# Optimization experiments

Measured on AMD Instinct MI355X. Metric: run time of the kernel, lower is better.

Reference implementation:

```python
import jax, jax.numpy as jnp
import numpy as np

H = 1024        # hidden_size
V = 50257       # output_size (vocab)
L = 2048        # max_length (encoder sequence)


def setup_inputs() -> dict:
    key = jax.random.key(0)
    ks = jax.random.split(key, 10)
    s = 1.0 / np.sqrt(H)
    return {
        "input_tok": jax.random.randint(ks[0], (1,), 0, V),
        "hidden": jax.random.normal(ks[1], (2, 1, H), dtype=jnp.float32),
        "encoder_hiddens": jax.random.normal(ks[2], (L, H), dtype=jnp.float32),
        # learned parameters
        "emb": jax.random.normal(ks[3], (V, H), dtype=jnp.float32),
        "W_ih": jax.random.uniform(ks[4], (2, H, H), jnp.float32, -s, s),   # per-direction input weights
        "W_hh": jax.random.uniform(ks[5], (2, H, H), jnp.float32, -s, s),   # per-direction recurrent weights
        "b_ih": jax.random.uniform(ks[6], (2, H), jnp.float32, -s, s),
        "b_hh": jax.random.uniform(ks[7], (2, H), jnp.float32, -s, s),
        "W_out": jax.random.uniform(ks[8], (V, 4 * H), jnp.float32, -s, s),
        "b_out": jax.random.uniform(ks[9], (V,), jnp.float32, -s, s),
    }


def reference(input_tok, hidden, encoder_hiddens, emb, W_ih, W_hh, b_ih, b_hh, W_out, b_out):
    # embedding lookup -> (H,)  (dropout is identity in eval mode)
    x = emb[input_tok[0]]
    # single-step bidirectional vanilla RNN cell (both directions see the same x):
    # h' = tanh(x W_ih^T + b_ih + h0 W_hh^T + b_hh), per direction d in {fwd, bwd}
    h0 = hidden[:, 0, :]                                    # (2, H)
    h = jnp.tanh(jnp.einsum('dho,o->dh', W_ih, x) + b_ih
                 + jnp.einsum('dho,do->dh', W_hh, h0) + b_hh)  # (2, H)
    # dot-product attention per direction over encoder states (L, H)
    energy = jnp.einsum('dh,lh->dl', h, encoder_hiddens)    # (2, L)
    attn = jax.nn.softmax(energy, axis=-1)                  # (2, L)
    attn_out = jnp.einsum('dl,lh->dh', attn, encoder_hiddens)  # (2, H)
    # concat: (attn_fwd, h_fwd, attn_bwd, h_bwd) -> (1, 4H)
    concat = jnp.concatenate([attn_out[0], h[0], attn_out[1], h[1]])[None, :]
    logits = concat @ W_out.T + b_out                       # (1, V)
    output = jax.nn.log_softmax(logits, axis=1)
    return output, h[:, None, :]                            # ((1, V), (2, 1, H))
```

## Files before the change

### kernel.cpp

```cpp
#include <hip/hip_runtime.h>
#include <cmath>

#define HDIM 1024
#define LSEQ 2048
#define VOCAB 50257

__device__ __forceinline__ float wave_sum(float v) {
#pragma unroll
    for (int off = 32; off; off >>= 1) v += __shfl_down(v, off, 64);
    return v;
}

__device__ __forceinline__ float wave_max(float v) {
#pragma unroll
    for (int off = 32; off; off >>= 1) v = fmaxf(v, __shfl_down(v, off, 64));
    return v;
}

__device__ __forceinline__ void lse_combine(float& m, float& s, float m2, float s2) {
    float nm = fmaxf(m, m2);
    s = s * expf(m - nm) + s2 * expf(m2 - nm);
    m = nm;
}

__global__ void rnn_kernel(const int* __restrict__ tok,
                           const float* __restrict__ hidden,
                           const float* __restrict__ emb,
                           const float* __restrict__ W_ih,
                           const float* __restrict__ W_hh,
                           const float* __restrict__ b_ih,
                           const float* __restrict__ b_hh,
                           float* __restrict__ concat,
                           float* __restrict__ out_h) {
    int wave = threadIdx.x >> 6, lane = threadIdx.x & 63;
    int row = blockIdx.x * 4 + wave;
    int d = row >> 10, i = row & 1023;
    int t = tok[0];
    const float* x  = emb + (size_t)t * HDIM;
    const float* h0 = hidden + d * HDIM;
    const float* wi = W_ih + (size_t)d * HDIM * HDIM + (size_t)i * HDIM;
    const float* wh = W_hh + (size_t)d * HDIM * HDIM + (size_t)i * HDIM;
    float acc = 0.f;
#pragma unroll
    for (int p = 0; p < 4; ++p) {
        int o = p * 256 + lane * 4;
        float4 a = *(const float4*)(wi + o);
        float4 b = *(const float4*)(x + o);
        acc += a.x * b.x + a.y * b.y + a.z * b.z + a.w * b.w;
        float4 c = *(const float4*)(wh + o);
        float4 e = *(const float4*)(h0 + o);
        acc += c.x * e.x + c.y * e.y + c.z * e.z + c.w * e.w;
    }
    acc = wave_sum(acc);
    if (lane == 0) {
        float hv = tanhf(acc + b_ih[d * HDIM + i] + b_hh[d * HDIM + i]);
        concat[d * 2048 + 1024 + i] = hv;
        out_h[d * HDIM + i] = hv;
    }
}

__global__ void energy_kernel(const float* __restrict__ enc,
                              const float* __restrict__ concat,
                              float* __restrict__ energy) {
    int wave = threadIdx.x >> 6, lane = threadIdx.x & 63;
    int row = blockIdx.x * 4 + wave;
    int d = row >> 11, l = row & 2047;
    const float* h  = concat + d * 2048 + 1024;
    const float* er = enc + (size_t)l * HDIM;
    float acc = 0.f;
#pragma unroll
    for (int p = 0; p < 4; ++p) {
        int o = p * 256 + lane * 4;
        float4 a = *(const float4*)(er + o);
        float4 b = *(const float4*)(h + o);
        acc += a.x * b.x + a.y * b.y + a.z * b.z + a.w * b.w;
    }
    acc = wave_sum(acc);
    if (lane == 0) energy[row] = acc;
}

__global__ void softmax_kernel(const float* __restrict__ energy,
                               float* __restrict__ attnw) {
    __shared__ float red[4];
    int d = blockIdx.x, t = threadIdx.x;
    int lane = t & 63, wave = t >> 6;
    const float* e = energy + d * LSEQ;
    float vals[8];
    float m = -1e30f;
#pragma unroll
    for (int k = 0; k < 8; ++k) { vals[k] = e[t + 256 * k]; m = fmaxf(m, vals[k]); }
    m = wave_max(m);
    if (lane == 0) red[wave] = m;
    __syncthreads();
    m = fmaxf(fmaxf(red[0], red[1]), fmaxf(red[2], red[3]));
    __syncthreads();
    float s = 0.f;
#pragma unroll
    for (int k = 0; k < 8; ++k) { vals[k] = expf(vals[k] - m); s += vals[k]; }
    s = wave_sum(s);
    if (lane == 0) red[wave] = s;
    __syncthreads();
    s = red[0] + red[1] + red[2] + red[3];
    float inv = 1.f / s;
#pragma unroll
    for (int k = 0; k < 8; ++k) attnw[d * LSEQ + t + 256 * k] = vals[k] * inv;
}

__global__ void attnout_partial_kernel(const float* __restrict__ enc,
                                       const float* __restrict__ attnw,
                                       float* __restrict__ part) {
    int b = blockIdx.x;
    int d = b >> 5, c = b & 31;
    int t = threadIdx.x;
    float acc0 = 0, acc1 = 0, acc2 = 0, acc3 = 0;
    const float* aw = attnw + d * LSEQ + c * 64;
    const float* e  = enc + (size_t)(c * 64) * HDIM;
    for (int l = 0; l < 64; ++l) {
        float a = aw[l];
        const float* row = e + (size_t)l * HDIM;
        acc0 += a * row[t];
        acc1 += a * row[t + 256];
        acc2 += a * row[t + 512];
        acc3 += a * row[t + 768];
    }
    float* pp = part + (size_t)b * HDIM;
    pp[t] = acc0; pp[t + 256] = acc1; pp[t + 512] = acc2; pp[t + 768] = acc3;
}

__global__ void attnout_reduce_kernel(const float* __restrict__ part,
                                      float* __restrict__ concat) {
    int idx = blockIdx.x * 256 + threadIdx.x;
    int d = idx >> 10, h = idx & 1023;
    float s = 0.f;
#pragma unroll 8
    for (int c = 0; c < 32; ++c) s += part[(size_t)(d * 32 + c) * HDIM + h];
    concat[d * 2048 + h] = s;
}

__global__ void logits_kernel(const float* __restrict__ W_out,
                              const float* __restrict__ b_out,
                              const float* __restrict__ concat,
                              float* __restrict__ logits) {
    int wave = threadIdx.x >> 6, lane = threadIdx.x & 63;
    int v = blockIdx.x * 4 + wave;
    if (v >= VOCAB) return;
    const float* w = W_out + (size_t)v * 4096;
    float acc = 0.f;
#pragma unroll
    for (int p = 0; p < 16; ++p) {
        int o = p * 256 + lane * 4;
        float4 a = *(const float4*)(w + o);
        float4 b = *(const float4*)(concat + o);
        acc += a.x * b.x + a.y * b.y + a.z * b.z + a.w * b.w;
    }
    acc = wave_sum(acc);
    if (lane == 0) logits[v] = acc + b_out[v];
}

__global__ void lse_partial_kernel(const float* __restrict__ logits,
                                   float* __restrict__ pm,
                                   float* __restrict__ ps) {
    __shared__ float rm[4], rs[4];
    int tid = blockIdx.x * 256 + threadIdx.x;
    float m = -1e30f, s = 0.f;
    for (int v = tid; v < VOCAB; v += 128 * 256) lse_combine(m, s, logits[v], 1.f);
    int lane = threadIdx.x & 63, wave = threadIdx.x >> 6;
#pragma unroll
    for (int off = 32; off; off >>= 1) {
        float m2 = __shfl_down(m, off, 64);
        float s2 = __shfl_down(s, off, 64);
        lse_combine(m, s, m2, s2);
    }
    if (lane == 0) { rm[wave] = m; rs[wave] = s; }
    __syncthreads();
    if (threadIdx.x == 0) {
        float fm = rm[0], fs = rs[0];
        for (int w = 1; w < 4; ++w) lse_combine(fm, fs, rm[w], rs[w]);
        pm[blockIdx.x] = fm;
        ps[blockIdx.x] = fs;
    }
}

__global__ void lse_final_kernel(const float* __restrict__ pm,
                                 const float* __restrict__ ps,
                                 float* __restrict__ Mval) {
    int lane = threadIdx.x;
    float m = pm[lane], s = ps[lane];
    lse_combine(m, s, pm[lane + 64], ps[lane + 64]);
#pragma unroll
    for (int off = 32; off; off >>= 1) {
        float m2 = __shfl_down(m, off, 64);
        float s2 = __shfl_down(s, off, 64);
        lse_combine(m, s, m2, s2);
    }
    if (lane == 0) Mval[0] = m + logf(s);
}

__global__ void sub_kernel(const float* __restrict__ logits,
                           const float* __restrict__ Mval,
                           float* __restrict__ out) {
    int v = blockIdx.x * 256 + threadIdx.x;
    if (v < VOCAB) out[v] = logits[v] - Mval[0];
}

extern "C" void kernel_launch(void* const* d_in, const int* in_sizes, int n_in,
                              void* d_out, int out_size, void* d_ws, size_t ws_size,
                              hipStream_t stream) {
    const int*   tok    = (const int*)d_in[0];
    const float* hidden = (const float*)d_in[1];
    const float* enc    = (const float*)d_in[2];
    const float* emb    = (const float*)d_in[3];
    const float* W_ih   = (const float*)d_in[4];
    const float* W_hh   = (const float*)d_in[5];
    const float* b_ih   = (const float*)d_in[6];
    const float* b_hh   = (const float*)d_in[7];
    const float* W_out  = (const float*)d_in[8];
    const float* b_out  = (const float*)d_in[9];
    float* out = (float*)d_out;

    float* ws     = (float*)d_ws;
    float* concat = ws;
    float* energy = ws + 4096;
    float* attnw  = ws + 8192;
    float* logits = ws + 12288;
    float* pm     = ws + 62592;
    float* ps     = ws + 62720;
    float* Mval   = ws + 62848;
    float* part   = ws + 62912;

    rnn_kernel<<<512, 256, 0, stream>>>(tok, hidden, emb, W_ih, W_hh, b_ih, b_hh,
                                        concat, out + VOCAB);
    energy_kernel<<<1024, 256, 0, stream>>>(enc, concat, energy);
    softmax_kernel<<<2, 256, 0, stream>>>(energy, attnw);
    attnout_partial_kernel<<<64, 256, 0, stream>>>(enc, attnw, part);
    attnout_reduce_kernel<<<8, 256, 0, stream>>>(part, concat);
    logits_kernel<<<(VOCAB + 3) / 4, 256, 0, stream>>>(W_out, b_out, concat, logits);
    lse_partial_kernel<<<128, 256, 0, stream>>>(logits, pm, ps);
    lse_final_kernel<<<1, 64, 0, stream>>>(pm, ps, Mval);
    sub_kernel<<<(VOCAB + 255) / 256, 256, 0, stream>>>(logits, Mval, out);
}
```

Baseline: 162.4 us.

## Fuse attention into flash-style split softmax and fold log-softmax reductions into logits

Replaces the separate energy, softmax, weighted-sum and reduce kernels with a chunked flash-attention kernel that computes local max/sum and unnormalised partial outputs, followed by a rescaling combine kernel. The logits kernel now also emits per-block max and exp-sum. A single output kernel has each block redundantly reduce those partials and subtract the log-sum-exp. This cuts the launch count and the intermediate buffer traffic, at the cost of redundant global LSE reduction in every output block.

Result: slower. 183.5 us (+13.0%).

```diff
diff --git a/kernel.cpp b/kernel.cpp
--- a/kernel.cpp
+++ b/kernel.cpp
@@ -4,16 +4,11 @@
 #define HDIM 1024
 #define LSEQ 2048
 #define VOCAB 50257
+#define LOGIT_BLOCKS ((VOCAB + 3) / 4)
 
 __device__ __forceinline__ float wave_sum(float v) {
 #pragma unroll
     for (int off = 32; off; off >>= 1) v += __shfl_down(v, off, 64);
-    return v;
-}
-
-__device__ __forceinline__ float wave_max(float v) {
-#pragma unroll
-    for (int off = 32; off; off >>= 1) v = fmaxf(v, __shfl_down(v, off, 64));
     return v;
 }
 
@@ -59,92 +54,83 @@
     }
 }
 
-__global__ void energy_kernel(const float* __restrict__ enc,
-                              const float* __restrict__ concat,
-                              float* __restrict__ energy) {
-    int wave = threadIdx.x >> 6, lane = threadIdx.x & 63;
-    int row = blockIdx.x * 4 + wave;
-    int d = row >> 11, l = row & 2047;
-    const float* h  = concat + d * 2048 + 1024;
-    const float* er = enc + (size_t)l * HDIM;
-    float acc = 0.f;
-#pragma unroll
-    for (int p = 0; p < 4; ++p) {
-        int o = p * 256 + lane * 4;
-        float4 a = *(const float4*)(er + o);
-        float4 b = *(const float4*)(h + o);
-        acc += a.x * b.x + a.y * b.y + a.z * b.z + a.w * b.w;
-    }
-    acc = wave_sum(acc);
-    if (lane == 0) energy[row] = acc;
-}
-
-__global__ void softmax_kernel(const float* __restrict__ energy,
-                               float* __restrict__ attnw) {
-    __shared__ float red[4];
-    int d = blockIdx.x, t = threadIdx.x;
-    int lane = t & 63, wave = t >> 6;
-    const float* e = energy + d * LSEQ;
-    float vals[8];
-    float m = -1e30f;
-#pragma unroll
-    for (int k = 0; k < 8; ++k) { vals[k] = e[t + 256 * k]; m = fmaxf(m, vals[k]); }
-    m = wave_max(m);
-    if (lane == 0) red[wave] = m;
-    __syncthreads();
-    m = fmaxf(fmaxf(red[0], red[1]), fmaxf(red[2], red[3]));
-    __syncthreads();
-    float s = 0.f;
-#pragma unroll
-    for (int k = 0; k < 8; ++k) { vals[k] = expf(vals[k] - m); s += vals[k]; }
-    s = wave_sum(s);
-    if (lane == 0) red[wave] = s;
-    __syncthreads();
-    s = red[0] + red[1] + red[2] + red[3];
-    float inv = 1.f / s;
-#pragma unroll
-    for (int k = 0; k < 8; ++k) attnw[d * LSEQ + t + 256 * k] = vals[k] * inv;
-}
-
-__global__ void attnout_partial_kernel(const float* __restrict__ enc,
-                                       const float* __restrict__ attnw,
-                                       float* __restrict__ part) {
+__global__ void flash_attn_kernel(const float* __restrict__ enc,
+                                  const float* __restrict__ concat,
+                                  float* __restrict__ part,
+                                  float* __restrict__ pm_a,
+                                  float* __restrict__ ps_a) {
+    __shared__ float e_sh[32];
     int b = blockIdx.x;
-    int d = b >> 5, c = b & 31;
-    int t = threadIdx.x;
+    int d = b >> 6, c = b & 63;
+    int t = threadIdx.x, wave = t >> 6, lane = t & 63;
+    int base = c * 32;
+    const float* h = concat + d * 2048 + 1024;
+
+    for (int r = 0; r < 8; ++r) {
+        int ll = wave * 8 + r;
+        const float* er = enc + (size_t)(base + ll) * HDIM;
+        float acc = 0.f;
+#pragma unroll
+        for (int p = 0; p < 4; ++p) {
+            int o = p * 256 + lane * 4;
+            float4 a = *(const float4*)(er + o);
+            float4 bb = *(const float4*)(h + o);
+            acc += a.x * bb.x + a.y * bb.y + a.z * bb.z + a.w * bb.w;
+        }
+        acc = wave_sum(acc);
+        if (lane == 0) e_sh[ll] = acc;
+    }
+    __syncthreads();
+
+    float m_c = -1e30f;
+#pragma unroll
+    for (int l = 0; l < 32; ++l) m_c = fmaxf(m_c, e_sh[l]);
+    float s_c = 0.f;
     float acc0 = 0, acc1 = 0, acc2 = 0, acc3 = 0;
-    const float* aw = attnw + d * LSEQ + c * 64;
-    const float* e  = enc + (size_t)(c * 64) * HDIM;
-    for (int l = 0; l < 64; ++l) {
-        float a = aw[l];
-        const float* row = e + (size_t)l * HDIM;
-        acc0 += a * row[t];
-        acc1 += a * row[t + 256];
-        acc2 += a * row[t + 512];
-        acc3 += a * row[t + 768];
+    for (int l = 0; l < 32; ++l) {
+        float p = expf(e_sh[l] - m_c);
+        s_c += p;
+        const float* row = enc + (size_t)(base + l) * HDIM;
+        acc0 += p * row[t];
+        acc1 += p * row[t + 256];
+        acc2 += p * row[t + 512];
+        acc3 += p * row[t + 768];
     }
     float* pp = part + (size_t)b * HDIM;
     pp[t] = acc0; pp[t + 256] = acc1; pp[t + 512] = acc2; pp[t + 768] = acc3;
-}
-
-__global__ void attnout_reduce_kernel(const float* __restrict__ part,
-                                      float* __restrict__ concat) {
+    if (t == 0) { pm_a[b] = m_c; ps_a[b] = s_c; }
+}
+
+__global__ void attn_combine_kernel(const float* __restrict__ part,
+                                    const float* __restrict__ pm_a,
+                                    const float* __restrict__ ps_a,
+                                    float* __restrict__ concat) {
     int idx = blockIdx.x * 256 + threadIdx.x;
     int d = idx >> 10, h = idx & 1023;
-    float s = 0.f;
-#pragma unroll 8
-    for (int c = 0; c < 32; ++c) s += part[(size_t)(d * 32 + c) * HDIM + h];
-    concat[d * 2048 + h] = s;
+    float M = -1e30f;
+    for (int c = 0; c < 64; ++c) M = fmaxf(M, pm_a[d * 64 + c]);
+    float S = 0.f, acc = 0.f;
+    for (int c = 0; c < 64; ++c) {
+        int cb = d * 64 + c;
+        float w = expf(pm_a[cb] - M);
+        S += ps_a[cb] * w;
+        acc += part[(size_t)cb * HDIM + h] * w;
+    }
+    concat[d * 2048 + h] = acc / S;
 }
 
 __global__ void logits_kernel(const float* __restrict__ W_out,
                               const float* __restrict__ b_out,
                               const float* __restrict__ concat,
-                              float* __restrict__ logits) {
+                              float* __restrict__ logits,
+                              float* __restrict__ pm,
+                              float* __restrict__ ps) {
+    __shared__ float lv[4];
     int wave = threadIdx.x >> 6, lane = threadIdx.x & 63;
     int v = blockIdx.x * 4 + wave;
-    if (v >= VOCAB) return;
-    const float* w = W_out + (size_t)v * 4096;
+    bool valid = v < VOCAB;
+    int vc = valid ? v : (VOCAB - 1);
+    const float* w = W_out + (size_t)vc * 4096;
     float acc = 0.f;
 #pragma unroll
     for (int p = 0; p < 16; ++p) {
@@ -154,17 +140,31 @@
         acc += a.x * b.x + a.y * b.y + a.z * b.z + a.w * b.w;
     }
     acc = wave_sum(acc);
-    if (lane == 0) logits[v] = acc + b_out[v];
-}
-
-__global__ void lse_partial_kernel(const float* __restrict__ logits,
-                                   float* __restrict__ pm,
-                                   float* __restrict__ ps) {
-    __shared__ float rm[4], rs[4];
-    int tid = blockIdx.x * 256 + threadIdx.x;
+    if (lane == 0) {
+        float val = acc + b_out[vc];
+        if (valid) logits[v] = val;
+        lv[wave] = valid ? val : -1e30f;
+    }
+    __syncthreads();
+    if (threadIdx.x == 0) {
+        float m = fmaxf(fmaxf(lv[0], lv[1]), fmaxf(lv[2], lv[3]));
+        float s = 0.f;
+#pragma unroll
+        for (int k = 0; k < 4; ++k)
+            if (lv[k] > -1e29f) s += expf(lv[k] - m);
+        pm[blockIdx.x] = m;
+        ps[blockIdx.x] = s;
+    }
+}
+
+__global__ void out_kernel(const float* __restrict__ logits,
+                           const float* __restrict__ pm,
+                           const float* __restrict__ ps,
+                           float* __restrict__ out) {
+    __shared__ float rm[4], rs[4], Msh;
+    int t = threadIdx.x, lane = t & 63, wave = t >> 6;
     float m = -1e30f, s = 0.f;
-    for (int v = tid; v < VOCAB; v += 128 * 256) lse_combine(m, s, logits[v], 1.f);
-    int lane = threadIdx.x & 63, wave = threadIdx.x >> 6;
+    for (int i = t; i < LOGIT_BLOCKS; i += 256) lse_combine(m, s, pm[i], ps[i]);
 #pragma unroll
     for (int off = 32; off; off >>= 1) {
         float m2 = __shfl_down(m, off, 64);
@@ -173,34 +173,15 @@
     }
     if (lane == 0) { rm[wave] = m; rs[wave] = s; }
     __syncthreads();
-    if (threadIdx.x == 0) {
+    if (t == 0) {
         float fm = rm[0], fs = rs[0];
-        for (int w = 1; w < 4; ++w) lse_combine(fm, fs, rm[w], rs[w]);
-        pm[blockIdx.x] = fm;
-        ps[blockIdx.x] = fs;
-    }
-}
-
-__global__ void lse_final_kernel(const float* __restrict__ pm,
-                                 const float* __restrict__ ps,
-                                 float* __restrict__ Mval) {
-    int lane = threadIdx.x;
-    float m = pm[lane], s = ps[lane];
-    lse_combine(m, s, pm[lane + 64], ps[lane + 64]);
-#pragma unroll
-    for (int off = 32; off; off >>= 1) {
-        float m2 = __shfl_down(m, off, 64);
-        float s2 = __shfl_down(s, off, 64);
-        lse_combine(m, s, m2, s2);
-    }
-    if (lane == 0) Mval[0] = m + logf(s);
-}
-
-__global__ void sub_kernel(const float* __restrict__ logits,
-                           const float* __restrict__ Mval,
-                           float* __restrict__ out) {
-    int v = blockIdx.x * 256 + threadIdx.x;
-    if (v < VOCAB) out[v] = logits[v] - Mval[0];
+        for (int k = 1; k < 4; ++k) lse_combine(fm, fs, rm[k], rs[k]);
+        Msh = fm + logf(fs);
+    }
+    __syncthreads();
+    float M = Msh;
+    int v = blockIdx.x * 256 + t;
+    if (v < VOCAB) out[v] = logits[v] - M;
 }
 
 extern "C" void kernel_launch(void* const* d_in, const int* in_sizes, int n_in,
@@ -220,22 +201,17 @@
 
     float* ws     = (float*)d_ws;
     float* concat = ws;
-    float* energy = ws + 4096;
-    float* attnw  = ws + 8192;
-    float* logits = ws + 12288;
-    float* pm     = ws + 62592;
-    float* ps     = ws + 62720;
-    float* Mval   = ws + 62848;
-    float* part   = ws + 62912;
+    float* pm_a   = ws + 4096;
+    float* ps_a   = ws + 4224;
+    float* pm     = ws + 4352;
+    float* ps     = ws + 16928;
+    float* part   = ws + 29504;
+    float* logits = ws + 29504;
 
     rnn_kernel<<<512, 256, 0, stream>>>(tok, hidden, emb, W_ih, W_hh, b_ih, b_hh,
                                         concat, out + VOCAB);
-    energy_kernel<<<1024, 256, 0, stream>>>(enc, concat, energy);
-    softmax_kernel<<<2, 256, 0, stream>>>(energy, attnw);
-    attnout_partial_kernel<<<64, 256, 0, stream>>>(enc, attnw, part);
-    attnout_reduce_kernel<<<8, 256, 0, stream>>>(part, concat);
-    logits_kernel<<<(VOCAB + 3) / 4, 256, 0, stream>>>(W_out, b_out, concat, logits);
-    lse_partial_kernel<<<128, 256, 0, stream>>>(logits, pm, ps);
-    lse_final_kernel<<<1, 64, 0, stream>>>(pm, ps, Mval);
-    sub_kernel<<<(VOCAB + 255) / 256, 256, 0, stream>>>(logits, Mval, out);
-}
+    flash_attn_kernel<<<128, 256, 0, stream>>>(enc, concat, part, pm_a, ps_a);
+    attn_combine_kernel<<<8, 256, 0, stream>>>(part, pm_a, ps_a, concat);
+    logits_kernel<<<LOGIT_BLOCKS, 256, 0, stream>>>(W_out, b_out, concat, logits, pm, ps);
+    out_kernel<<<(VOCAB + 255) / 256, 256, 0, stream>>>(logits, pm, ps, out);
+}
```
